# Kernel optimization log

Hardware: AMD Instinct MI355X
Metric: run time of the kernel (lower is better)

The kernel has to match this reference:

```python
import jax, jax.numpy as jnp
import numpy as np

N_SITES = 1024
A_PER_SITE = 2
R_PER_ALLELE = 16
N_ALLELES = N_SITES * A_PER_SITE
N_READS = N_ALLELES * R_PER_ALLELE
C_IN, C, L = 16, 32, 150


def conv1d(x, w, stride=1, dilation=1, pad=2):
    return jax.lax.conv_general_dilated(
        x, w, (stride,), [(pad, pad)], rhs_dilation=(dilation,),
        dimension_numbers=('NCH', 'OIH', 'NCH'))


def reduce_slots(d, slots):
    # cumsum-diff segmented sum over dim 0, exactly as torch reduceSlots
    res = jnp.cumsum(d, axis=0)
    idx = jnp.cumsum(slots) - 1
    sel = res[idx]
    padded = jnp.concatenate([jnp.zeros_like(sel[:1]), sel[:-1]], axis=0)
    return sel - padded


def xattn(allele, site0, site1, wq, wk, wv, wo):
    # cross-attention: allele features query the two expanded site-feature streams
    q = jnp.einsum('oc,ncl->nol', wq, allele)
    kv = jnp.concatenate([site0, site1], axis=-1)  # [Na, C, 2*L']
    k = jnp.einsum('oc,ncl->nol', wk, kv)
    v = jnp.einsum('oc,ncl->nol', wv, kv)
    scores = jnp.einsum('ncl,ncm->nlm', q, k) / np.float32(np.sqrt(C))
    ctx = jnp.einsum('nlm,ncm->ncl', jax.nn.softmax(scores, axis=-1), v)
    return jnp.mean(allele + ctx, axis=-1) @ wo.T  # [Na, 2]


def setup_inputs():
    ks = jax.random.split(jax.random.key(0), 24)
    w = lambda i, shape: jax.random.normal(ks[i], shape, jnp.float32) * 0.05
    return {
        'tensors0': jax.random.normal(ks[0], (N_READS, C_IN, L), jnp.float32),
        'tensors1': jax.random.normal(ks[1], (N_READS, C_IN, L), jnp.float32),
        'conv0_w': w(2, (C, C_IN, 5)), 'conv1_w': w(3, (C, C_IN, 5)),
        'comp0_w': w(4, (C, C, 3)), 'comp1_w': w(5, (C, C, 3)), 'comp2_w': w(6, (C, C, 3)),
        'xq0': w(7, (C, C)), 'xk0': w(8, (C, C)), 'xv0': w(9, (C, C)), 'xo0': w(10, (2, C)),
        'xq1': w(11, (C, C)), 'xk1': w(12, (C, C)), 'xv1': w(13, (C, C)), 'xo1': w(14, (2, C)),
        'xq2': w(15, (C, C)), 'xk2': w(16, (C, C)), 'xv2': w(17, (C, C)), 'xo2': w(18, (2, C)),
        'comb_w': w(19, (C, 2 * C)), 'meta_w': w(20, (3, 2 * C)), 'meta_b': w(21, (3,)),
        'num_alleles_per_site': jnp.full((N_SITES,), A_PER_SITE, jnp.int32),
        'num_reads0': jnp.full((N_ALLELES,), R_PER_ALLELE, jnp.int32),
        'num_reads1': jnp.full((N_ALLELES,), R_PER_ALLELE, jnp.int32),
    }


def reference(tensors0, tensors1, conv0_w, conv1_w, comp0_w, comp1_w, comp2_w,
              xq0, xk0, xv0, xo0, xq1, xk1, xv1, xo1, xq2, xk2, xv2, xo2,
              comb_w, meta_w, meta_b, num_alleles_per_site, num_reads0, num_reads1):
    compressor = lambda x, w: jax.nn.relu(conv1d(x, w, stride=2, dilation=2, pad=2))

    def compress_and_predict(red_allele, comp_w, xw):
        cfa = compressor(red_allele, comp_w)                       # [Na, C, L']
        rfs = reduce_slots(red_allele, num_alleles_per_site)       # [Ns, C, L]
        cfs0 = compressor(rfs, comp_w)                             # [Ns, C, L']
        exp0 = jnp.repeat(cfs0, num_alleles_per_site, axis=0, total_repeat_length=N_ALLELES)
        cfs1 = reduce_slots(cfa, num_alleles_per_site)             # [Ns, C, L']
        exp1 = jnp.repeat(cfs1, num_alleles_per_site, axis=0, total_repeat_length=N_ALLELES)
        return xattn(cfa, exp0, exp1, *xw), (cfs0, cfs1)

    rc0 = jax.nn.relu(conv1d(tensors0, conv0_w, pad=2))            # [Nr, C, L]
    red0 = reduce_slots(rc0, num_reads0)                           # [Na, C, L]
    e0, _ = compress_and_predict(red0, comp0_w, (xq0, xk0, xv0, xo0))

    rc1 = jax.nn.relu(conv1d(tensors1, conv1_w, pad=2))
    red1 = reduce_slots(rc1, num_reads1)
    e1, _ = compress_and_predict(red1, comp1_w, (xq1, xk1, xv1, xo1))

    red2 = jax.nn.relu(jnp.einsum('oc,ncl->nol', comb_w, jnp.concatenate([red0, red1], axis=1)))
    e2, (s0, s1) = compress_and_predict(red2, comp2_w, (xq2, xk2, xv2, xo2))

    meta_feat = jnp.mean(jnp.concatenate([s0, s1], axis=1), axis=-1)  # [Ns, 2C]
    meta = jax.nn.softmax(meta_feat @ meta_w.T + meta_b, axis=-1)     # [Ns, 3]
    return (jnp.stack([e0, e1, e2]), meta)
```

## Files before the change

kernel.cpp:

```cpp
#include <hip/hip_runtime.h>
#include <math.h>

#define NS 1024
#define NA 2048
#define CIN 16
#define CC 32
#define LL 150
#define LC 75

typedef __attribute__((ext_vector_type(8))) short short8;
typedef __attribute__((ext_vector_type(4))) float float4v;

__device__ __forceinline__ unsigned short f2bf(float f) {
  unsigned int u = __float_as_uint(f);
  unsigned int r = (u + 0x7FFFu + ((u >> 16) & 1u)) >> 16;
  return (unsigned short)r;
}

__device__ __forceinline__ unsigned int pkbf(float lo, float hi) {
  return (unsigned int)f2bf(lo) | ((unsigned int)f2bf(hi) << 16);
}

__global__ __launch_bounds__(256) void k_conv_sum_mfma(const float* __restrict__ x,
                                                       const float* __restrict__ w,
                                                       float* __restrict__ red) {
  __shared__ unsigned short xs[2][154 * 32];
  const int a = blockIdx.x;
  const int tid = threadIdx.x;
  const int lane = tid & 63;
  const int wv = tid >> 6;

  short8 afr[2][3];
  {
    const int mrow = lane & 15;
    const int h = lane >> 4;
    for (int mt = 0; mt < 2; ++mt) {
      const int c = mt * 16 + mrow;
      for (int s = 0; s < 3; ++s) {
        short8 f;
#pragma unroll
        for (int j = 0; j < 8; ++j) {
          int ic = 4 * h + (j >> 1);
          int tap = 2 * s + (j & 1);
          float wval = (tap < 5) ? w[c * 80 + ic * 5 + tap] : 0.f;
          f[j] = (short)f2bf(wval);
        }
        afr[mt][s] = f;
      }
    }
  }

  float4v sum[2][3];
#pragma unroll
  for (int mt = 0; mt < 2; ++mt)
#pragma unroll
    for (int nt = 0; nt < 3; ++nt) sum[mt][nt] = (float4v)(0.f);

  const int nbase = wv * 48;
  const int nrow = lane & 15;
  const int hh = lane >> 4;
  const float4v zf = (float4v)(0.f);

  auto stage = [&](int r, int buf) {
    const float* xr = x + (size_t)(a * 16 + r) * (CIN * LL);
    unsigned int* xb32 = (unsigned int*)xs[buf];
    for (int idx = tid; idx < 16 * 38; idx += 256) {
      const int ic = idx & 15;
      const int seg = idx >> 4;
      const int l0 = seg * 4;
      const float* row = xr + ic * LL;
      float v0, v1, v2, v3, v4;
      if (seg < 37) {
        float2 u = *(const float2*)(row + l0);
        float2 u2 = *(const float2*)(row + l0 + 2);
        v0 = u.x; v1 = u.y; v2 = u2.x; v3 = u2.y;
        v4 = row[l0 + 4];
      } else {
        float2 u = *(const float2*)(row + 148);
        v0 = u.x; v1 = u.y; v2 = 0.f; v3 = 0.f; v4 = 0.f;
      }
      const int hb = 4 * (ic >> 2) + (ic & 3);
      unsigned int* b32 = xb32 + 16 * (l0 + 2) + hb;
      b32[0]  = pkbf(v0, v1);
      b32[16] = pkbf(v1, v2);
      b32[32] = pkbf(v2, v3);
      b32[48] = pkbf(v3, v4);
    }
    if (tid < 32) {
      const int ic = tid & 15;
      const int which = tid >> 4;
      const int hb = 4 * (ic >> 2) + (ic & 3);
      xb32[16 * which + hb] = which ? pkbf(0.f, xr[ic * LL]) : 0u;
    }
  };

  stage(0, 0);
  __syncthreads();

  for (int r = 0; r < 16; ++r) {
    const int cur = r & 1;
    if (r + 1 < 16) stage(r + 1, cur ^ 1);

    float4v acc[2][3];
#pragma unroll
    for (int s = 0; s < 3; ++s) {
#pragma unroll
      for (int nt = 0; nt < 3; ++nt) {
        int p = nbase + nt * 16 + nrow + 2 * s;
        if (p >= 154) p -= 154;
        short8 bfrag = *(const short8*)&xs[cur][(4 * p + hh) * 8];
#pragma unroll
        for (int mt = 0; mt < 2; ++mt) {
          acc[mt][nt] = __builtin_amdgcn_mfma_f32_16x16x32_bf16(
              afr[mt][s], bfrag, (s == 0) ? zf : acc[mt][nt], 0, 0, 0);
        }
      }
    }
#pragma unroll
    for (int mt = 0; mt < 2; ++mt)
#pragma unroll
      for (int nt = 0; nt < 3; ++nt)
#pragma unroll
        for (int q = 0; q < 4; ++q) sum[mt][nt][q] += fmaxf(acc[mt][nt][q], 0.f);

    __syncthreads();
  }

  const int ccol = lane & 15;
  const int crow4 = (lane >> 4) * 4;
  for (int mt = 0; mt < 2; ++mt)
    for (int nt = 0; nt < 3; ++nt) {
      int l = nbase + nt * 16 + ccol;
      if (l < LL) {
#pragma unroll
        for (int q = 0; q < 4; ++q) {
          int c = mt * 16 + crow4 + q;
          red[(size_t)a * (CC * LL) + c * LL + l] = sum[mt][nt][q];
        }
      }
    }
}

__global__ __launch_bounds__(256) void k_comb(const float* __restrict__ red0,
                                              const float* __restrict__ red1,
                                              const float* __restrict__ cw,
                                              float* __restrict__ out) {
  __shared__ float ins[64][152];
  __shared__ float cwl[64][CC];
  const int a = blockIdx.x;
  const int tid = threadIdx.x;

  for (int i = tid; i < 64 * CC; i += 256) {
    int c = i & 31; int c2 = i >> 5;
    cwl[c2][c] = cw[c * 64 + c2];
  }
  for (int i = tid; i < CC * LL; i += 256) {
    int c2 = i / LL; int l = i - c2 * LL;
    ins[c2][l] = red0[(size_t)a * (CC * LL) + i];
    ins[32 + c2][l] = red1[(size_t)a * (CC * LL) + i];
  }
  __syncthreads();

  const int c = tid & 31;
  const int lg = tid >> 5;
  const int l0 = lg * 19;
  const int nl = (LL - l0 < 19) ? (LL - l0) : 19;
  float v[19];
#pragma unroll
  for (int j = 0; j < 19; ++j) v[j] = 0.f;
  for (int c2 = 0; c2 < 64; ++c2) {
    float wv = cwl[c2][c];
#pragma unroll
    for (int j = 0; j < 19; ++j) v[j] += wv * ins[c2][l0 + j];
  }
  float* o = out + (size_t)a * (CC * LL) + c * LL + l0;
  for (int j = 0; j < nl; ++j) o[j] = fmaxf(v[j], 0.f);
}

__global__ __launch_bounds__(256) void k_compress2(const float* __restrict__ src,
                                                   const float* __restrict__ w,
                                                   float* __restrict__ cfa,
                                                   float* __restrict__ cfs) {
  __shared__ float ins0[CC][164];
  __shared__ float ins1[CC][164];
  __shared__ float ws[CC][3][CC];
  const int sfull = blockIdx.x;
  const int tid = threadIdx.x;

  for (int i = tid; i < CC * 3 * CC; i += 256) {
    int c = i & 31; int kk = i >> 5; int ic = kk / 3; int t = kk - ic * 3;
    ws[ic][t][c] = w[c * (CC * 3) + ic * 3 + t];
  }
  if (tid < CC) {
    ins0[tid][0] = 0.f; ins0[tid][1] = 0.f; ins0[tid][152] = 0.f; ins0[tid][153] = 0.f;
    ins1[tid][0] = 0.f; ins1[tid][1] = 0.f; ins1[tid][152] = 0.f; ins1[tid][153] = 0.f;
  }
  {
    const float* s0 = src + (size_t)(2 * sfull) * (CC * LL);
    const float* s1 = s0 + CC * LL;
    for (int i = tid; i < CC * LL; i += 256) {
      int ic = i / LL; int l = i - ic * LL;
      ins0[ic][l + 2] = s0[i];
      ins1[ic][l + 2] = s1[i];
    }
  }
  __syncthreads();

  const int c = tid & 31;
  const int jg = tid >> 5;
  const int j0 = jg * 10;
  const int nj = (LC - j0 < 10) ? (LC - j0) : 10;
  float v0[10], v1[10];
#pragma unroll
  for (int j = 0; j < 10; ++j) { v0[j] = 0.f; v1[j] = 0.f; }
  for (int ic = 0; ic < CC; ++ic) {
    float w0 = ws[ic][0][c], w1 = ws[ic][1][c], w2 = ws[ic][2][c];
    float xa[12], xb[12];
#pragma unroll
    for (int i = 0; i < 12; ++i) {
      xa[i] = ins0[ic][2 * j0 + 2 * i];
      xb[i] = ins1[ic][2 * j0 + 2 * i];
    }
#pragma unroll
    for (int j = 0; j < 10; ++j) {
      v0[j] += w0 * xa[j] + w1 * xa[j + 1] + w2 * xa[j + 2];
      v1[j] += w0 * xb[j] + w1 * xb[j + 1] + w2 * xb[j + 2];
    }
  }
  float* oa0 = cfa + (size_t)(2 * sfull) * (CC * LC) + c * LC + j0;
  float* oa1 = oa0 + CC * LC;
  float* os  = cfs + (size_t)sfull * (CC * LC) + c * LC + j0;
  for (int j = 0; j < nj; ++j) {
    float a0 = v0[j], a1 = v1[j];
    oa0[j] = fmaxf(a0, 0.f);
    oa1[j] = fmaxf(a1, 0.f);
    os[j]  = fmaxf(a0 + a1, 0.f);
  }
}

#define BKV   0
#define BWK   4800
#define BWV   5856
#define BWQ   6912
#define BQT   7968
#define BCF   10368
#define BKB   10368
#define BVB   15232
#define BROWP 0
#define BPART 6080
#define BMS   6592
#define ARENA 20224

__device__ __forceinline__ void attn_phase_d(float* __restrict__ ar, int g, int t,
                                             float& ms) {
  const float scale = 0.17677669529663687f;
  const int rbase = BROWP + g * 760;
#pragma unroll 1
  for (int cc = 0; cc < 2; ++cc) {
    const int ch = g + 8 * cc;
    if (ch >= 15) break;
    const int r0 = ch * 5;

    float2 acc[5][3];
#pragma unroll
    for (int i = 0; i < 5; ++i)
#pragma unroll
      for (int u = 0; u < 3; ++u) acc[i][u] = make_float2(0.f, 0.f);

#pragma unroll 1
    for (int c2 = 0; c2 < 32; c2 += 2) {
      float2 q01[5];
#pragma unroll
      for (int i = 0; i < 5; ++i) q01[i] = *(const float2*)&ar[BQT + (r0 + i) * 32 + c2];
      const int cb0 = BKB + c2 * 152 + 2 * t;
      const int cb1 = cb0 + 152;
      float2 ka0 = *(const float2*)&ar[cb0];
      float2 ka1 = *(const float2*)&ar[cb0 + 64];
      float2 ka2 = *(const float2*)&ar[cb0 + 128];
      float2 kb0 = *(const float2*)&ar[cb1];
      float2 kb1 = *(const float2*)&ar[cb1 + 64];
      float2 kb2 = *(const float2*)&ar[cb1 + 128];
#pragma unroll
      for (int i = 0; i < 5; ++i) {
        acc[i][0].x += q01[i].x * ka0.x + q01[i].y * kb0.x;
        acc[i][0].y += q01[i].x * ka0.y + q01[i].y * kb0.y;
        acc[i][1].x += q01[i].x * ka1.x + q01[i].y * kb1.x;
        acc[i][1].y += q01[i].x * ka1.y + q01[i].y * kb1.y;
        acc[i][2].x += q01[i].x * ka2.x + q01[i].y * kb2.x;
        acc[i][2].y += q01[i].x * ka2.y + q01[i].y * kb2.y;
      }
    }

    float inv[5];
#pragma unroll
    for (int i = 0; i < 5; ++i) {
      float s0x = acc[i][0].x * scale, s0y = acc[i][0].y * scale;
      float s1x = acc[i][1].x * scale, s1y = acc[i][1].y * scale;
      float s2x = acc[i][2].x * scale, s2y = acc[i][2].y * scale;
      if (t >= 11) { s2x = -1e30f; s2y = -1e30f; }
      float mx = fmaxf(fmaxf(fmaxf(s0x, s0y), fmaxf(s1x, s1y)), fmaxf(s2x, s2y));
#pragma unroll
      for (int off = 16; off > 0; off >>= 1) mx = fmaxf(mx, __shfl_xor(mx, off, 32));
      float p0x = __expf(s0x - mx), p0y = __expf(s0y - mx);
      float p1x = __expf(s1x - mx), p1y = __expf(s1y - mx);
      float p2x = __expf(s2x - mx), p2y = __expf(s2y - mx);
      float ss = p0x + p0y + p1x + p1y + p2x + p2y;
#pragma unroll
      for (int off = 16; off > 0; off >>= 1) ss += __shfl_xor(ss, off, 32);
      inv[i] = 1.f / ss;
      const int rb = rbase + i * 152 + 2 * t;
      *(float2*)&ar[rb]      = make_float2(p0x, p0y);
      *(float2*)&ar[rb + 64] = make_float2(p1x, p1y);
      if (t <= 11) *(float2*)&ar[rb + 128] = make_float2(p2x, p2y);
    }

    float pv[5] = {0.f, 0.f, 0.f, 0.f, 0.f};
    for (int mq = 0; mq < 38; ++mq) {
      float4 vv = *(const float4*)&ar[BVB + t * 156 + 4 * mq];
#pragma unroll
      for (int i = 0; i < 5; ++i) {
        float4 pp = *(const float4*)&ar[rbase + i * 152 + 4 * mq];
        pv[i] += pp.x * vv.x + pp.y * vv.y + pp.z * vv.z + pp.w * vv.w;
      }
    }
#pragma unroll
    for (int i = 0; i < 5; ++i) ms += pv[i] * inv[i];
  }
}

__global__ __launch_bounds__(256) void k_attn(const float* __restrict__ cfa,
                                              const float* __restrict__ cfs0,
                                              const float* __restrict__ wq,
                                              const float* __restrict__ wk,
                                              const float* __restrict__ wv,
                                              const float* __restrict__ wo,
                                              float* __restrict__ eout) {
  __shared__ float ar[ARENA];
  const int s = blockIdx.x;
  const int tid = threadIdx.x;
  const int g = tid >> 5;
  const int t = tid & 31;

  const float* a0g = cfa + (size_t)(2 * s) * (CC * LC);
  const float* a1g = a0g + CC * LC;

  for (int i = tid; i < CC * CC; i += 256) {
    int o = i >> 5, ii = i & 31;
    ar[BWQ + ii * 33 + o] = wq[i];
    ar[BWK + ii * 33 + o] = wk[i];
    ar[BWV + ii * 33 + o] = wv[i];
  }
  {
    const float* sg = cfs0 + (size_t)s * (CC * LC);
    for (int i = tid; i < CC * LC; i += 256) {
      int c = i / 75, l = i - c * 75;
      float v0 = a0g[i], v1 = a1g[i];
      ar[BKV + c * 150 + l]      = sg[i];
      ar[BKV + c * 150 + 75 + l] = v0 + v1;
      ar[BCF + c * 77 + l]       = v0;
    }
  }
  __syncthreads();

  float cfp0 = 0.f;
  {
    float wqc[32];
#pragma unroll
    for (int ii = 0; ii < 32; ++ii) wqc[ii] = ar[BWQ + ii * 33 + t];
    for (int row = g; row < 75; row += 8) {
      float acc = 0.f;
#pragma unroll
      for (int ii = 0; ii < 32; ++ii) acc += wqc[ii] * ar[BCF + ii * 77 + row];
      ar[BQT + row * 32 + t] = acc;
      cfp0 += ar[BCF + t * 77 + row];
    }
  }
  __syncthreads();

  {
    float wkc[32], wvc[32];
#pragma unroll
    for (int ii = 0; ii < 32; ++ii) {
      wkc[ii] = ar[BWK + ii * 33 + t];
      wvc[ii] = ar[BWV + ii * 33 + t];
    }
    for (int idx = tid; idx < CC * LL; idx += 256) {
      int o = idx & 31, m = idx >> 5;
      float ka = 0.f, va = 0.f;
#pragma unroll
      for (int ii = 0; ii < 32; ++ii) {
        float x = ar[BKV + ii * 150 + m];
        ka += wkc[ii] * x;
        va += wvc[ii] * x;
      }
      ar[BKB + o * 152 + m] = ka;
      ar[BVB + o * 156 + m] = va;
    }
    if (tid < 64) ar[BVB + (tid >> 1) * 156 + 150 + (tid & 1)] = 0.f;
  }
  __syncthreads();

  float ms0 = 0.f;
  attn_phase_d(ar, g, t, ms0);
  __syncthreads();

  float cfp1 = 0.f;
  {
    float wqc[32];
#pragma unroll
    for (int ii = 0; ii < 32; ++ii) wqc[ii] = ar[BWQ + ii * 33 + t];
    for (int row = g; row < 75; row += 8) {
      float acc = 0.f;
#pragma unroll
      for (int ii = 0; ii < 32; ++ii) acc += wqc[ii] * a1g[ii * 75 + row];
      ar[BQT + row * 32 + t] = acc;
      cfp1 += a1g[t * 75 + row];
    }
  }
  __syncthreads();

  float ms1 = 0.f;
  attn_phase_d(ar, g, t, ms1);

  ar[BPART + g * 32 + t]       = cfp0 + ms0;
  ar[BPART + 256 + g * 32 + t] = cfp1 + ms1;
  __syncthreads();

  if (tid < 64) {
    int al = tid >> 5, tt = tid & 31;
    float tot = 0.f;
#pragma unroll
    for (int gg = 0; gg < 8; ++gg) tot += ar[BPART + al * 256 + gg * 32 + tt];
    ar[BMS + al * 32 + tt] = tot * (1.f / 75.f);
  }
  __syncthreads();
  if (tid < 4) {
    int al = tid >> 1, o2 = tid & 1;
    float e = 0.f;
#pragma unroll
    for (int c2 = 0; c2 < CC; ++c2) e += wo[o2 * CC + c2] * ar[BMS + al * 32 + c2];
    eout[s * 4 + tid] = e;
  }
}

__global__ __launch_bounds__(64) void k_meta(const float* __restrict__ cfs0,
                                             const float* __restrict__ cfa2,
                                             const float* __restrict__ mw,
                                             const float* __restrict__ mb,
                                             float* __restrict__ mout) {
  __shared__ float feat[64];
  __shared__ float lgt[3];
  const int s = blockIdx.x;
  const int tid = threadIdx.x;
  float f = 0.f;
  if (tid < 32) {
    const float* p = cfs0 + (size_t)s * (CC * LC) + tid * LC;
    for (int l = 0; l < LC; ++l) f += p[l];
  } else {
    const float* p0 = cfa2 + (size_t)(2 * s) * (CC * LC) + (tid - 32) * LC;
    const float* p1 = cfa2 + (size_t)(2 * s + 1) * (CC * LC) + (tid - 32) * LC;
    for (int l = 0; l < LC; ++l) f += p0[l] + p1[l];
  }
  feat[tid] = f * (1.f / 75.f);
  __syncthreads();
  if (tid < 3) {
    float acc2 = mb[tid];
    for (int c2 = 0; c2 < 64; ++c2) acc2 += mw[tid * 64 + c2] * feat[c2];
    lgt[tid] = acc2;
  }
  __syncthreads();
  if (tid < 3) {
    float mx = fmaxf(lgt[0], fmaxf(lgt[1], lgt[2]));
    float e0 = __expf(lgt[0] - mx), e1 = __expf(lgt[1] - mx), e2 = __expf(lgt[2] - mx);
    mout[s * 3 + tid] = __expf(lgt[tid] - mx) / (e0 + e1 + e2);
  }
}

extern "C" void kernel_launch(void* const* d_in, const int* in_sizes, int n_in,
                              void* d_out, int out_size, void* d_ws, size_t ws_size,
                              hipStream_t stream) {
  const float* t0      = (const float*)d_in[0];
  const float* t1      = (const float*)d_in[1];
  const float* conv0_w = (const float*)d_in[2];
  const float* conv1_w = (const float*)d_in[3];
  const float* comp0_w = (const float*)d_in[4];
  const float* comp1_w = (const float*)d_in[5];
  const float* comp2_w = (const float*)d_in[6];
  const float* xq0 = (const float*)d_in[7];
  const float* xk0 = (const float*)d_in[8];
  const float* xv0 = (const float*)d_in[9];
  const float* xo0 = (const float*)d_in[10];
  const float* xq1 = (const float*)d_in[11];
  const float* xk1 = (const float*)d_in[12];
  const float* xv1 = (const float*)d_in[13];
  const float* xo1 = (const float*)d_in[14];
  const float* xq2 = (const float*)d_in[15];
  const float* xk2 = (const float*)d_in[16];
  const float* xv2 = (const float*)d_in[17];
  const float* xo2 = (const float*)d_in[18];
  const float* comb_w = (const float*)d_in[19];
  const float* meta_w = (const float*)d_in[20];
  const float* meta_b = (const float*)d_in[21];

  float* wsf  = (float*)d_ws;
  float* red0 = wsf;
  float* red1 = red0 + (size_t)NA * CC * LL;
  float* cfa  = red1 + (size_t)NA * CC * LL;
  float* cfs0 = cfa + (size_t)NA * CC * LC;
  float* out  = (float*)d_out;

  k_conv_sum_mfma<<<NA, 256, 0, stream>>>(t0, conv0_w, red0);
  k_conv_sum_mfma<<<NA, 256, 0, stream>>>(t1, conv1_w, red1);

  k_compress2<<<NS, 256, 0, stream>>>(red0, comp0_w, cfa, cfs0);
  k_attn<<<NS, 256, 0, stream>>>(cfa, cfs0, xq0, xk0, xv0, xo0, out + 0);

  k_compress2<<<NS, 256, 0, stream>>>(red1, comp1_w, cfa, cfs0);
  k_attn<<<NS, 256, 0, stream>>>(cfa, cfs0, xq1, xk1, xv1, xo1, out + 2 * NA);

  k_comb<<<NA, 256, 0, stream>>>(red0, red1, comb_w, red0);
  k_compress2<<<NS, 256, 0, stream>>>(red0, comp2_w, cfa, cfs0);
  k_attn<<<NS, 256, 0, stream>>>(cfa, cfs0, xq2, xk2, xv2, xo2, out + 4 * NA);

  k_meta<<<NS, 64, 0, stream>>>(cfs0, cfa, meta_w, meta_b, out + 6 * NA);
}
```

Baseline: 1.398 ms.

## Fuse strided compressor conv into cross-attention kernel and skip unused global writes

Merges the compressor convolution kernel into the attention kernel. The compressed allele and site features are written straight into the shared-memory arena the attention uses, so the global write and re-read of cfa/cfs between two launches goes away. For the first two passes only the second allele's features are written to global memory. The full cfa/cfs writes needed by the meta kernel are kept only for the final pass, controlled by a flag. This saves three launches and a round trip through global memory per pass, at the cost of a longer single kernel that reuses the arena for both phases.

Result: faster. 1.361 ms (-2.6%).

```diff
diff --git a/kernel.cpp b/kernel.cpp
--- a/kernel.cpp
+++ b/kernel.cpp
@@ -177,67 +177,6 @@
   for (int j = 0; j < nl; ++j) o[j] = fmaxf(v[j], 0.f);
 }
 
-__global__ __launch_bounds__(256) void k_compress2(const float* __restrict__ src,
-                                                   const float* __restrict__ w,
-                                                   float* __restrict__ cfa,
-                                                   float* __restrict__ cfs) {
-  __shared__ float ins0[CC][164];
-  __shared__ float ins1[CC][164];
-  __shared__ float ws[CC][3][CC];
-  const int sfull = blockIdx.x;
-  const int tid = threadIdx.x;
-
-  for (int i = tid; i < CC * 3 * CC; i += 256) {
-    int c = i & 31; int kk = i >> 5; int ic = kk / 3; int t = kk - ic * 3;
-    ws[ic][t][c] = w[c * (CC * 3) + ic * 3 + t];
-  }
-  if (tid < CC) {
-    ins0[tid][0] = 0.f; ins0[tid][1] = 0.f; ins0[tid][152] = 0.f; ins0[tid][153] = 0.f;
-    ins1[tid][0] = 0.f; ins1[tid][1] = 0.f; ins1[tid][152] = 0.f; ins1[tid][153] = 0.f;
-  }
-  {
-    const float* s0 = src + (size_t)(2 * sfull) * (CC * LL);
-    const float* s1 = s0 + CC * LL;
-    for (int i = tid; i < CC * LL; i += 256) {
-      int ic = i / LL; int l = i - ic * LL;
-      ins0[ic][l + 2] = s0[i];
-      ins1[ic][l + 2] = s1[i];
-    }
-  }
-  __syncthreads();
-
-  const int c = tid & 31;
-  const int jg = tid >> 5;
-  const int j0 = jg * 10;
-  const int nj = (LC - j0 < 10) ? (LC - j0) : 10;
-  float v0[10], v1[10];
-#pragma unroll
-  for (int j = 0; j < 10; ++j) { v0[j] = 0.f; v1[j] = 0.f; }
-  for (int ic = 0; ic < CC; ++ic) {
-    float w0 = ws[ic][0][c], w1 = ws[ic][1][c], w2 = ws[ic][2][c];
-    float xa[12], xb[12];
-#pragma unroll
-    for (int i = 0; i < 12; ++i) {
-      xa[i] = ins0[ic][2 * j0 + 2 * i];
-      xb[i] = ins1[ic][2 * j0 + 2 * i];
-    }
-#pragma unroll
-    for (int j = 0; j < 10; ++j) {
-      v0[j] += w0 * xa[j] + w1 * xa[j + 1] + w2 * xa[j + 2];
-      v1[j] += w0 * xb[j] + w1 * xb[j + 1] + w2 * xb[j + 2];
-    }
-  }
-  float* oa0 = cfa + (size_t)(2 * sfull) * (CC * LC) + c * LC + j0;
-  float* oa1 = oa0 + CC * LC;
-  float* os  = cfs + (size_t)sfull * (CC * LC) + c * LC + j0;
-  for (int j = 0; j < nj; ++j) {
-    float a0 = v0[j], a1 = v1[j];
-    oa0[j] = fmaxf(a0, 0.f);
-    oa1[j] = fmaxf(a1, 0.f);
-    os[j]  = fmaxf(a0 + a1, 0.f);
-  }
-}
-
 #define BKV   0
 #define BWK   4800
 #define BWV   5856
@@ -250,6 +189,9 @@
 #define BPART 6080
 #define BMS   6592
 #define ARENA 20224
+#define FIN0  0
+#define FIN1  5248
+#define FWS   10496
 
 __device__ __forceinline__ void attn_phase_d(float* __restrict__ ar, int g, int t,
                                              float& ms) {
@@ -328,37 +270,89 @@
   }
 }
 
-__global__ __launch_bounds__(256) void k_attn(const float* __restrict__ cfa,
-                                              const float* __restrict__ cfs0,
-                                              const float* __restrict__ wq,
-                                              const float* __restrict__ wk,
-                                              const float* __restrict__ wv,
-                                              const float* __restrict__ wo,
-                                              float* __restrict__ eout) {
+__global__ __launch_bounds__(256) void k_cattn(const float* __restrict__ red,
+                                               const float* __restrict__ cw,
+                                               const float* __restrict__ wq,
+                                               const float* __restrict__ wk,
+                                               const float* __restrict__ wv,
+                                               const float* __restrict__ wo,
+                                               float* __restrict__ cfa,
+                                               float* __restrict__ cfs,
+                                               float* __restrict__ eout,
+                                               int wg) {
   __shared__ float ar[ARENA];
   const int s = blockIdx.x;
   const int tid = threadIdx.x;
   const int g = tid >> 5;
   const int t = tid & 31;
 
-  const float* a0g = cfa + (size_t)(2 * s) * (CC * LC);
-  const float* a1g = a0g + CC * LC;
-
+  float* a0g = cfa + (size_t)(2 * s) * (CC * LC);
+  float* a1g = a0g + CC * LC;
+  float* sgw = cfs + (size_t)s * (CC * LC);
+
+  for (int i = tid; i < CC * 3 * CC; i += 256) {
+    int c = i & 31; int kk = i >> 5;
+    ar[FWS + kk * 32 + c] = cw[c * (CC * 3) + kk];
+  }
+  if (tid < CC) {
+    ar[FIN0 + tid * 164 + 0] = 0.f; ar[FIN0 + tid * 164 + 1] = 0.f;
+    ar[FIN0 + tid * 164 + 152] = 0.f; ar[FIN0 + tid * 164 + 153] = 0.f;
+    ar[FIN1 + tid * 164 + 0] = 0.f; ar[FIN1 + tid * 164 + 1] = 0.f;
+    ar[FIN1 + tid * 164 + 152] = 0.f; ar[FIN1 + tid * 164 + 153] = 0.f;
+  }
+  {
+    const float* s0 = red + (size_t)(2 * s) * (CC * LL);
+    const float* s1 = s0 + CC * LL;
+    for (int i = tid; i < CC * LL; i += 256) {
+      int ic = i / LL; int l = i - ic * LL;
+      ar[FIN0 + ic * 164 + l + 2] = s0[i];
+      ar[FIN1 + ic * 164 + l + 2] = s1[i];
+    }
+  }
+  __syncthreads();
+
+  const int j0 = g * 10;
+  const int nj = (LC - j0 < 10) ? (LC - j0) : 10;
+  float v0[10], v1[10];
+#pragma unroll
+  for (int j = 0; j < 10; ++j) { v0[j] = 0.f; v1[j] = 0.f; }
+  for (int ic = 0; ic < CC; ++ic) {
+    float w0 = ar[FWS + (ic * 3 + 0) * 32 + t];
+    float w1 = ar[FWS + (ic * 3 + 1) * 32 + t];
+    float w2 = ar[FWS + (ic * 3 + 2) * 32 + t];
+    float xa[12], xb[12];
+#pragma unroll
+    for (int i = 0; i < 12; ++i) {
+      xa[i] = ar[FIN0 + ic * 164 + 2 * j0 + 2 * i];
+      xb[i] = ar[FIN1 + ic * 164 + 2 * j0 + 2 * i];
+    }
+#pragma unroll
+    for (int j = 0; j < 10; ++j) {
+      v0[j] += w0 * xa[j] + w1 * xa[j + 1] + w2 * xa[j + 2];
+      v1[j] += w0 * xb[j] + w1 * xb[j + 1] + w2 * xb[j + 2];
+    }
+  }
+  __syncthreads();
+
+  for (int j = 0; j < nj; ++j) {
+    const int jj = j0 + j;
+    float r0 = fmaxf(v0[j], 0.f);
+    float r1 = fmaxf(v1[j], 0.f);
+    float cs = fmaxf(v0[j] + v1[j], 0.f);
+    ar[BKV + t * 150 + jj]      = cs;
+    ar[BKV + t * 150 + 75 + jj] = r0 + r1;
+    ar[BCF + t * 77 + jj]       = r0;
+    a1g[t * 75 + jj] = r1;
+    if (wg) {
+      a0g[t * 75 + jj] = r0;
+      sgw[t * 75 + jj] = cs;
+    }
+  }
   for (int i = tid; i < CC * CC; i += 256) {
     int o = i >> 5, ii = i & 31;
     ar[BWQ + ii * 33 + o] = wq[i];
     ar[BWK + ii * 33 + o] = wk[i];
     ar[BWV + ii * 33 + o] = wv[i];
-  }
-  {
-    const float* sg = cfs0 + (size_t)s * (CC * LC);
-    for (int i = tid; i < CC * LC; i += 256) {
-      int c = i / 75, l = i - c * 75;
-      float v0 = a0g[i], v1 = a1g[i];
-      ar[BKV + c * 150 + l]      = sg[i];
-      ar[BKV + c * 150 + 75 + l] = v0 + v1;
-      ar[BCF + c * 77 + l]       = v0;
-    }
   }
   __syncthreads();
 
@@ -512,15 +506,14 @@
   k_conv_sum_mfma<<<NA, 256, 0, stream>>>(t0, conv0_w, red0);
   k_conv_sum_mfma<<<NA, 256, 0, stream>>>(t1, conv1_w, red1);
 
-  k_compress2<<<NS, 256, 0, stream>>>(red0, comp0_w, cfa, cfs0);
-  k_attn<<<NS, 256, 0, stream>>>(cfa, cfs0, xq0, xk0, xv0, xo0, out + 0);
-
-  k_compress2<<<NS, 256, 0, stream>>>(red1, comp1_w, cfa, cfs0);
-  k_attn<<<NS, 256, 0, stream>>>(cfa, cfs0, xq1, xk1, xv1, xo1, out + 2 * NA);
+  k_cattn<<<NS, 256, 0, stream>>>(red0, comp0_w, xq0, xk0, xv0, xo0,
+                                  cfa, cfs0, out + 0, 0);
+  k_cattn<<<NS, 256, 0, stream>>>(red1, comp1_w, xq1, xk1, xv1, xo1,
+                                  cfa, cfs0, out + 2 * NA, 0);
 
   k_comb<<<NA, 256, 0, stream>>>(red0, red1, comb_w, red0);
-  k_compress2<<<NS, 256, 0, stream>>>(red0, comp2_w, cfa, cfs0);
-  k_attn<<<NS, 256, 0, stream>>>(cfa, cfs0, xq2, xk2, xv2, xo2, out + 4 * NA);
+  k_cattn<<<NS, 256, 0, stream>>>(red0, comp2_w, xq2, xk2, xv2, xo2,
+                                  cfa, cfs0, out + 4 * NA, 1);
 
   k_meta<<<NS, 64, 0, stream>>>(cfs0, cfa, meta_w, meta_b, out + 6 * NA);
 }
```
